# Performance work log

Measured on AMD Instinct MI355X. Metric: run time of the kernel, lower is better.

The kernel has to match this reference:

```python
import jax, jax.numpy as jnp
import numpy as np

B, D, HIST = 32768, 128, 30     # batch, d_model, history length
M, H, RANK = 15, 4, 8           # memory_length, d_hidden, operator max_rank


def spectral_op(W, sigma_scale, sigma_shift, alpha, residual_scale):
    """W' = alpha * (U diag(f(S)) Vh) + residual_scale * W, f(S)=softplus(scale)*S+shift.
    W: (h, d) 2D matrix (h=4 < RANK so k = h and no tail singular values remain)."""
    U, S, Vh = jnp.linalg.svd(W, full_matrices=False)   # U:(h,h) S:(h,) Vh:(h,d)
    k = min(RANK, S.shape[-1])
    scale = jax.nn.softplus(sigma_scale[:k])
    S_new = scale * S[:k] + sigma_shift[:k]
    if S.shape[-1] > k:
        S_new = jnp.concatenate([S_new, S[k:]], axis=-1)
    W_spec = (U * S_new[None, :]) @ Vh
    return alpha * W_spec + residual_scale * W


def setup_inputs() -> dict:
    key = jax.random.key(0)
    k0, k1 = jax.random.split(key)
    return {
        "pre_acts_history": jax.random.normal(k0, (B, D, HIST), jnp.float32),
        "weights_1": jax.random.normal(k1, (M, H, D), jnp.float32) * 0.02,
        "bias_1": jnp.zeros((1, H, D), jnp.float32),
        "bias_2": jnp.zeros((1, H, D), jnp.float32),
        "bias_3": jnp.zeros((1, D), jnp.float32),
        "contract_weights": jnp.ones((M,), jnp.float32) / M,
        "sigma_scale": jnp.ones((RANK,), jnp.float32),
        "sigma_shift": jnp.zeros((RANK,), jnp.float32),
        "alpha": jnp.full((1,), 0.7, jnp.float32),          # 1 - residual_blend
        "residual_scale": jnp.full((1,), 0.3, jnp.float32),  # residual_blend
    }


def reference(pre_acts_history, weights_1, bias_1, bias_2, bias_3,
              contract_weights, sigma_scale, sigma_shift, alpha, residual_scale):
    a = alpha[0]
    r = residual_scale[0]
    inputs = pre_acts_history[..., -M:]                         # (B, D, M)
    # layer 1: per-d contraction over memory
    h1 = jnp.einsum('bdM,Mhd->bdh', inputs, weights_1)
    h1 = jax.nn.relu(h1 + jnp.transpose(bias_1, (0, 2, 1)))     # (B, D, H)
    # derive W2 = T(contract(W1)), W3 = T(W2)
    w = jax.nn.softmax(contract_weights)
    W1_c = jnp.einsum('m,mhd->hd', w, weights_1)                # (H, D)
    W2 = spectral_op(W1_c, sigma_scale, sigma_shift, a, r)      # (H, D)
    # layer 2: elementwise gating ('bdh,hd->bdh')
    h2 = jax.nn.relu(h1 * W2.T[None] + jnp.transpose(bias_2, (0, 2, 1)))
    W3 = spectral_op(W2, sigma_scale, sigma_shift, a, r)        # (H, D)
    out = jnp.einsum('bdh,hd->bd', h2, W3) + bias_3             # (B, D)
    return out
```

## Files before the change

kernel.cpp:

```cpp
#include <hip/hip_runtime.h>
#include <math.h>

#define B_N    32768
#define D_N    128
#define HIST_N 30
#define M_N    15
#define H_N    4

#define TILE_ROWS   512
#define TILE_FLOATS (TILE_ROWS * HIST_N)
#define TILE_F4     (TILE_FLOATS / 4)
#define WAVE_F4     480
#define WAVE_FLOATS (WAVE_F4 * 4)
#define NBLOCKS     256
#define NTHREADS    512
#define TPB         (B_N * D_N / TILE_ROWS / NBLOCKS)

typedef float f32x4 __attribute__((ext_vector_type(4)));

__global__ __launch_bounds__(NTHREADS, 1) void fused_kernel(
        const float* __restrict__ pa,
        const float* __restrict__ w1,
        const float* __restrict__ b1,
        const float* __restrict__ b2,
        const float* __restrict__ b3,
        const float* __restrict__ cw,
        const float* __restrict__ ss,
        const float* __restrict__ sh,
        const float* __restrict__ al,
        const float* __restrict__ rs,
        float* __restrict__ out) {
    const int tid   = threadIdx.x;
    const int lane  = tid & 63;
    const int wv_id = tid >> 6;
    const int d     = tid & 127;

    __shared__ __align__(16) f32x4 lds4[2][TILE_F4];
    __shared__ float W1c[H_N][D_N];
    __shared__ float Gsh[16];
    __shared__ float Msh[32];

    const f32x4* pa4 = (const f32x4*)pa;
    const size_t tile0 = (size_t)blockIdx.x * TPB;

#define LOAD_SET(v0,v1,v2,v3,v4,v5,v6,v7,t) do {                          \
        const f32x4* s_ = pa4 + (size_t)(t) * TILE_F4 + wv_id * WAVE_F4;  \
        v0 = __builtin_nontemporal_load(s_ + lane);                       \
        v1 = __builtin_nontemporal_load(s_ + 64 + lane);                  \
        v2 = __builtin_nontemporal_load(s_ + 128 + lane);                 \
        v3 = __builtin_nontemporal_load(s_ + 192 + lane);                 \
        v4 = __builtin_nontemporal_load(s_ + 256 + lane);                 \
        v5 = __builtin_nontemporal_load(s_ + 320 + lane);                 \
        v6 = __builtin_nontemporal_load(s_ + 384 + lane);                 \
        if (lane < 32) v7 = __builtin_nontemporal_load(s_ + 448 + lane);  \
    } while (0)

#define WRITE_SET(v0,v1,v2,v3,v4,v5,v6,v7,buf) do {                    \
        f32x4* L_ = &lds4[buf][0] + wv_id * WAVE_F4;                   \
        L_[lane] = v0;        L_[64 + lane] = v1;                      \
        L_[128 + lane] = v2;  L_[192 + lane] = v3;                     \
        L_[256 + lane] = v4;  L_[320 + lane] = v5;                     \
        L_[384 + lane] = v6;                                           \
        if (lane < 32) L_[448 + lane] = v7;                            \
    } while (0)

    f32x4 a0, a1, a2, a3, a4, a5, a6, a7;
    f32x4 b0, b1r, b2r, b3r, b4, b5, b6, b7;
    a7 = (f32x4){0.f, 0.f, 0.f, 0.f};
    b7 = (f32x4){0.f, 0.f, 0.f, 0.f};

    LOAD_SET(a0, a1, a2, a3, a4, a5, a6, a7, tile0);
    LOAD_SET(b0, b1r, b2r, b3r, b4, b5, b6, b7, tile0 + 1);

    float wv[M_N][H_N];
#pragma unroll
    for (int m = 0; m < M_N; ++m)
#pragma unroll
        for (int h = 0; h < H_N; ++h)
            wv[m][h] = w1[(m * H_N + h) * D_N + d];

    float b1v[H_N], b2v[H_N];
#pragma unroll
    for (int h = 0; h < H_N; ++h) {
        b1v[h] = b1[h * D_N + d];
        b2v[h] = b2[h * D_N + d];
    }
    const float b3v = b3[d];

    float swm[M_N];
    {
        float mx = cw[0];
#pragma unroll
        for (int m = 1; m < M_N; ++m) mx = fmaxf(mx, cw[m]);
        float s = 0.f;
#pragma unroll
        for (int m = 0; m < M_N; ++m) { swm[m] = expf(cw[m] - mx); s += swm[m]; }
        float inv = 1.f / s;
#pragma unroll
        for (int m = 0; m < M_N; ++m) swm[m] *= inv;
    }

    if (tid < 128) {
#pragma unroll
        for (int h = 0; h < H_N; ++h) {
            float acc = 0.f;
#pragma unroll
            for (int m = 0; m < M_N; ++m)
                acc = fmaf(swm[m], w1[(m * H_N + h) * D_N + tid], acc);
            W1c[h][tid] = acc;
        }
    }
    asm volatile("s_waitcnt lgkmcnt(0)" ::: "memory");
    __builtin_amdgcn_s_barrier();

    if (tid < 16) {
        const int i = tid >> 2, j = tid & 3;
        float s = 0.f;
        for (int st = 0; st < 128; ++st) {
            int dd = (st + tid * 8) & 127;
            s = fmaf(W1c[i][dd], W1c[j][dd], s);
        }
        Gsh[tid] = s;
    }
    asm volatile("s_waitcnt lgkmcnt(0)" ::: "memory");
    __builtin_amdgcn_s_barrier();

    if (tid == 0) {
        float G[4][4], U[4][4];
#pragma unroll
        for (int i = 0; i < 4; ++i)
#pragma unroll
            for (int j = 0; j < 4; ++j) {
                G[i][j] = Gsh[i * 4 + j];
                U[i][j] = (i == j) ? 1.f : 0.f;
            }
        for (int sweep = 0; sweep < 6; ++sweep)
            for (int p = 0; p < 3; ++p)
                for (int q = p + 1; q < 4; ++q) {
                    float apq = G[p][q];
                    if (fabsf(apq) < 1e-30f) continue;
                    float theta = (G[q][q] - G[p][p]) / (2.f * apq);
                    float t = ((theta >= 0.f) ? 1.f : -1.f) /
                              (fabsf(theta) + sqrtf(theta * theta + 1.f));
                    float c = 1.f / sqrtf(t * t + 1.f), sn = t * c;
                    for (int i = 0; i < 4; ++i) {
                        float gip = G[i][p], giq = G[i][q];
                        G[i][p] = c * gip - sn * giq;
                        G[i][q] = sn * gip + c * giq;
                    }
                    for (int i = 0; i < 4; ++i) {
                        float gpi = G[p][i], gqi = G[q][i];
                        G[p][i] = c * gpi - sn * gqi;
                        G[q][i] = sn * gpi + c * gqi;
                    }
                    for (int i = 0; i < 4; ++i) {
                        float uip = U[i][p], uiq = U[i][q];
                        U[i][p] = c * uip - sn * uiq;
                        U[i][q] = sn * uip + c * uiq;
                    }
                }
        float lam[4];
#pragma unroll
        for (int i = 0; i < 4; ++i) lam[i] = G[i][i];
        int ord[4] = {0, 1, 2, 3};
        for (int i = 0; i < 4; ++i)
            for (int j = i + 1; j < 4; ++j)
                if (lam[ord[j]] > lam[ord[i]]) { int t2 = ord[i]; ord[i] = ord[j]; ord[j] = t2; }

        const float a = al[0], r = rs[0];
        float c1[4], S2a[4];
        for (int p = 0; p < 4; ++p) {
            int e = ord[p];
            float S = sqrtf(fmaxf(lam[e], 0.f));
            float x = ss[p];
            float sp = (x > 20.f) ? x : log1pf(expf(x));
            float ratio = (S > 1e-30f) ? ((sp * S + sh[p]) / S) : sp;
            c1[e] = a * ratio + r;
            S2a[e] = fabsf(c1[e]) * S;
        }
        int ord2[4] = {0, 1, 2, 3};
        for (int i = 0; i < 4; ++i)
            for (int j = i + 1; j < 4; ++j)
                if (S2a[ord2[j]] > S2a[ord2[i]]) { int t2 = ord2[i]; ord2[i] = ord2[j]; ord2[j] = t2; }
        float c12[4];
        for (int p = 0; p < 4; ++p) {
            int e = ord2[p];
            float Sa = S2a[e];
            float x = ss[p];
            float sp = (x > 20.f) ? x : log1pf(expf(x));
            float ratio2 = (Sa > 1e-30f) ? ((sp * Sa + sh[p]) / Sa) : sp;
            c12[e] = (a * ratio2 + r) * c1[e];
        }
#pragma unroll
        for (int i = 0; i < 4; ++i)
#pragma unroll
            for (int j = 0; j < 4; ++j) {
                float m2 = 0.f, m3 = 0.f;
#pragma unroll
                for (int e = 0; e < 4; ++e) {
                    float uu = U[i][e] * U[j][e];
                    m2 = fmaf(uu, c1[e], m2);
                    m3 = fmaf(uu, c12[e], m3);
                }
                Msh[i * 4 + j] = m2;
                Msh[16 + i * 4 + j] = m3;
            }
    }
    asm volatile("s_waitcnt lgkmcnt(0)" ::: "memory");
    __builtin_amdgcn_s_barrier();

    float w2v[H_N], w3v[H_N];
#pragma unroll
    for (int h = 0; h < H_N; ++h) {
        float s2 = 0.f, s3 = 0.f;
#pragma unroll
        for (int k4 = 0; k4 < 4; ++k4) {
            float wc = W1c[k4][d];
            s2 = fmaf(Msh[h * 4 + k4], wc, s2);
            s3 = fmaf(Msh[16 + h * 4 + k4], wc, s3);
        }
        w2v[h] = s2;
        w3v[h] = s3;
    }

    const int rd_base = wv_id * WAVE_FLOATS + lane * HIST_N + (HIST_N - M_N);

    auto compute_tile = [&](int buf, size_t t) {
        const float* L = (const float*)&lds4[buf][0] + rd_base;
        float x0 = L[0];
        float h1[H_N];
#pragma unroll
        for (int h = 0; h < H_N; ++h) h1[h] = x0 * wv[0][h];
#pragma unroll
        for (int c = 0; c < 7; ++c) {
            float2 q = *(const float2*)(L + 1 + 2 * c);
#pragma unroll
            for (int h = 0; h < H_N; ++h) h1[h] = fmaf(q.x, wv[1 + 2 * c][h], h1[h]);
#pragma unroll
            for (int h = 0; h < H_N; ++h) h1[h] = fmaf(q.y, wv[2 + 2 * c][h], h1[h]);
        }
        float acc = b3v;
#pragma unroll
        for (int h = 0; h < H_N; ++h) {
            float v = fmaxf(h1[h] + b1v[h], 0.f);
            float u = fmaxf(fmaf(v, w2v[h], b2v[h]), 0.f);
            acc = fmaf(u, w3v[h], acc);
        }
        out[t * TILE_ROWS + wv_id * 64 + lane] = acc;
    };

    for (int k = 0; k < TPB; k += 2) {
        if (k == 0) asm volatile("s_waitcnt vmcnt(8)" ::: "memory");
        else        asm volatile("s_waitcnt vmcnt(9)" ::: "memory");
        WRITE_SET(a0, a1, a2, a3, a4, a5, a6, a7, 0);
        asm volatile("s_waitcnt lgkmcnt(0)" ::: "memory");
        compute_tile(0, tile0 + k);
        if (k + 2 < TPB) LOAD_SET(a0, a1, a2, a3, a4, a5, a6, a7, tile0 + k + 2);

        if (k + 1 == TPB - 1) asm volatile("s_waitcnt vmcnt(0)" ::: "memory");
        else                  asm volatile("s_waitcnt vmcnt(9)" ::: "memory");
        WRITE_SET(b0, b1r, b2r, b3r, b4, b5, b6, b7, 1);
        asm volatile("s_waitcnt lgkmcnt(0)" ::: "memory");
        compute_tile(1, tile0 + k + 1);
        if (k + 3 < TPB) LOAD_SET(b0, b1r, b2r, b3r, b4, b5, b6, b7, tile0 + k + 3);
    }
#undef LOAD_SET
#undef WRITE_SET
}

extern "C" void kernel_launch(void* const* d_in, const int* in_sizes, int n_in,
                              void* d_out, int out_size, void* d_ws, size_t ws_size,
                              hipStream_t stream) {
    const float* pa = (const float*)d_in[0];
    const float* w1 = (const float*)d_in[1];
    const float* b1 = (const float*)d_in[2];
    const float* b2 = (const float*)d_in[3];
    const float* b3 = (const float*)d_in[4];
    const float* cw = (const float*)d_in[5];
    const float* ss = (const float*)d_in[6];
    const float* sh = (const float*)d_in[7];
    const float* al = (const float*)d_in[8];
    const float* rs = (const float*)d_in[9];
    float* out = (float*)d_out;

    fused_kernel<<<NBLOCKS, NTHREADS, 0, stream>>>(pa, w1, b1, b2, b3, cw, ss, sh, al, rs, out);
}
```

Measured before the change: 109.4 us.

## Double block threads so each wave loads and computes half as many rows

Raises the block to 1024 threads (16 waves). Each wave now stages 32 rows of history per tile instead of 64, so the per-thread register footprint for in-flight loads is halved and more waves issue memory requests in parallel. Only half the lanes of each wave do the compute and store, and the vmcnt wait counts are adjusted to the smaller load set. The trade-off is idle half-waves during compute and more threads sharing the same per-block setup work.

```diff
diff --git a/kernel.cpp b/kernel.cpp
--- a/kernel.cpp
+++ b/kernel.cpp
@@ -10,10 +10,11 @@
 #define TILE_ROWS   512
 #define TILE_FLOATS (TILE_ROWS * HIST_N)
 #define TILE_F4     (TILE_FLOATS / 4)
-#define WAVE_F4     480
+#define WAVE_ROWS   32
+#define WAVE_F4     240
 #define WAVE_FLOATS (WAVE_F4 * 4)
 #define NBLOCKS     256
-#define NTHREADS    512
+#define NTHREADS    1024
 #define TPB         (B_N * D_N / TILE_ROWS / NBLOCKS)
 
 typedef float f32x4 __attribute__((ext_vector_type(4)));
@@ -33,7 +34,8 @@
     const int tid   = threadIdx.x;
     const int lane  = tid & 63;
     const int wv_id = tid >> 6;
-    const int d     = tid & 127;
+    const int row_g = wv_id * WAVE_ROWS + (lane & (WAVE_ROWS - 1));
+    const int d     = row_g & (D_N - 1);
 
     __shared__ __align__(16) f32x4 lds4[2][TILE_F4];
     __shared__ float W1c[H_N][D_N];
@@ -43,34 +45,28 @@
     const f32x4* pa4 = (const f32x4*)pa;
     const size_t tile0 = (size_t)blockIdx.x * TPB;
 
-#define LOAD_SET(v0,v1,v2,v3,v4,v5,v6,v7,t) do {                          \
+#define LOAD_SET(v0,v1,v2,v3,t) do {                                      \
         const f32x4* s_ = pa4 + (size_t)(t) * TILE_F4 + wv_id * WAVE_F4;  \
         v0 = __builtin_nontemporal_load(s_ + lane);                       \
         v1 = __builtin_nontemporal_load(s_ + 64 + lane);                  \
         v2 = __builtin_nontemporal_load(s_ + 128 + lane);                 \
-        v3 = __builtin_nontemporal_load(s_ + 192 + lane);                 \
-        v4 = __builtin_nontemporal_load(s_ + 256 + lane);                 \
-        v5 = __builtin_nontemporal_load(s_ + 320 + lane);                 \
-        v6 = __builtin_nontemporal_load(s_ + 384 + lane);                 \
-        if (lane < 32) v7 = __builtin_nontemporal_load(s_ + 448 + lane);  \
+        if (lane < 48) v3 = __builtin_nontemporal_load(s_ + 192 + lane);  \
     } while (0)
 
-#define WRITE_SET(v0,v1,v2,v3,v4,v5,v6,v7,buf) do {                    \
+#define WRITE_SET(v0,v1,v2,v3,buf) do {                                \
         f32x4* L_ = &lds4[buf][0] + wv_id * WAVE_F4;                   \
         L_[lane] = v0;        L_[64 + lane] = v1;                      \
-        L_[128 + lane] = v2;  L_[192 + lane] = v3;                     \
-        L_[256 + lane] = v4;  L_[320 + lane] = v5;                     \
-        L_[384 + lane] = v6;                                           \
-        if (lane < 32) L_[448 + lane] = v7;                            \
+        L_[128 + lane] = v2;                                           \
+        if (lane < 48) L_[192 + lane] = v3;                            \
     } while (0)
 
-    f32x4 a0, a1, a2, a3, a4, a5, a6, a7;
-    f32x4 b0, b1r, b2r, b3r, b4, b5, b6, b7;
-    a7 = (f32x4){0.f, 0.f, 0.f, 0.f};
-    b7 = (f32x4){0.f, 0.f, 0.f, 0.f};
-
-    LOAD_SET(a0, a1, a2, a3, a4, a5, a6, a7, tile0);
-    LOAD_SET(b0, b1r, b2r, b3r, b4, b5, b6, b7, tile0 + 1);
+    f32x4 a0, a1, a2, a3;
+    f32x4 b0, b1r, b2r, b3r;
+    a3 = (f32x4){0.f, 0.f, 0.f, 0.f};
+    b3r = (f32x4){0.f, 0.f, 0.f, 0.f};
+
+    LOAD_SET(a0, a1, a2, a3, tile0);
+    LOAD_SET(b0, b1r, b2r, b3r, tile0 + 1);
 
     float wv[M_N][H_N];
 #pragma unroll
@@ -223,46 +219,50 @@
         w3v[h] = s3;
     }
 
-    const int rd_base = wv_id * WAVE_FLOATS + lane * HIST_N + (HIST_N - M_N);
+    const bool active = (lane < WAVE_ROWS);
+    const int rd_base = wv_id * WAVE_FLOATS + (lane & (WAVE_ROWS - 1)) * HIST_N
+                      + (HIST_N - M_N);
 
     auto compute_tile = [&](int buf, size_t t) {
-        const float* L = (const float*)&lds4[buf][0] + rd_base;
-        float x0 = L[0];
-        float h1[H_N];
-#pragma unroll
-        for (int h = 0; h < H_N; ++h) h1[h] = x0 * wv[0][h];
-#pragma unroll
-        for (int c = 0; c < 7; ++c) {
-            float2 q = *(const float2*)(L + 1 + 2 * c);
-#pragma unroll
-            for (int h = 0; h < H_N; ++h) h1[h] = fmaf(q.x, wv[1 + 2 * c][h], h1[h]);
-#pragma unroll
-            for (int h = 0; h < H_N; ++h) h1[h] = fmaf(q.y, wv[2 + 2 * c][h], h1[h]);
-        }
-        float acc = b3v;
-#pragma unroll
-        for (int h = 0; h < H_N; ++h) {
-            float v = fmaxf(h1[h] + b1v[h], 0.f);
-            float u = fmaxf(fmaf(v, w2v[h], b2v[h]), 0.f);
-            acc = fmaf(u, w3v[h], acc);
-        }
-        out[t * TILE_ROWS + wv_id * 64 + lane] = acc;
+        if (active) {
+            const float* L = (const float*)&lds4[buf][0] + rd_base;
+            float x0 = L[0];
+            float h1[H_N];
+#pragma unroll
+            for (int h = 0; h < H_N; ++h) h1[h] = x0 * wv[0][h];
+#pragma unroll
+            for (int c = 0; c < 7; ++c) {
+                float2 q = *(const float2*)(L + 1 + 2 * c);
+#pragma unroll
+                for (int h = 0; h < H_N; ++h) h1[h] = fmaf(q.x, wv[1 + 2 * c][h], h1[h]);
+#pragma unroll
+                for (int h = 0; h < H_N; ++h) h1[h] = fmaf(q.y, wv[2 + 2 * c][h], h1[h]);
+            }
+            float acc = b3v;
+#pragma unroll
+            for (int h = 0; h < H_N; ++h) {
+                float v = fmaxf(h1[h] + b1v[h], 0.f);
+                float u = fmaxf(fmaf(v, w2v[h], b2v[h]), 0.f);
+                acc = fmaf(u, w3v[h], acc);
+            }
+            out[t * TILE_ROWS + row_g] = acc;
+        }
     };
 
     for (int k = 0; k < TPB; k += 2) {
-        if (k == 0) asm volatile("s_waitcnt vmcnt(8)" ::: "memory");
-        else        asm volatile("s_waitcnt vmcnt(9)" ::: "memory");
-        WRITE_SET(a0, a1, a2, a3, a4, a5, a6, a7, 0);
+        if (k == 0) asm volatile("s_waitcnt vmcnt(4)" ::: "memory");
+        else        asm volatile("s_waitcnt vmcnt(5)" ::: "memory");
+        WRITE_SET(a0, a1, a2, a3, 0);
         asm volatile("s_waitcnt lgkmcnt(0)" ::: "memory");
         compute_tile(0, tile0 + k);
-        if (k + 2 < TPB) LOAD_SET(a0, a1, a2, a3, a4, a5, a6, a7, tile0 + k + 2);
+        if (k + 2 < TPB) LOAD_SET(a0, a1, a2, a3, tile0 + k + 2);
 
         if (k + 1 == TPB - 1) asm volatile("s_waitcnt vmcnt(0)" ::: "memory");
-        else                  asm volatile("s_waitcnt vmcnt(9)" ::: "memory");
-        WRITE_SET(b0, b1r, b2r, b3r, b4, b5, b6, b7, 1);
+        else                  asm volatile("s_waitcnt vmcnt(5)" ::: "memory");
+        WRITE_SET(b0, b1r, b2r, b3r, 1);
         asm volatile("s_waitcnt lgkmcnt(0)" ::: "memory");
         compute_tile(1, tile0 + k + 1);
-        if (k + 3 < TPB) LOAD_SET(b0, b1r, b2r, b3r, b4, b5, b6, b7, tile0 + k + 3);
+        if (k + 3 < TPB) LOAD_SET(b0, b1r, b2r, b3r, tile0 + k + 3);
     }
 #undef LOAD_SET
 #undef WRITE_SET
```

Measured after the change: 150.9 us. 1.38x slower.
